# Optimization experiments

Hardware: AMD Instinct MI355X
Metric: run time of the kernel (lower is better)

## Reference

```python
import jax, jax.numpy as jnp
import numpy as np

H = 64
W = 64
MOVES = 15          # ring expansion steps in make_weight_map
THRESHOLD = 5       # self.threshold
BG_WEIGHT = 10.0    # default weight outside the rings


def make_weight_map(kp):
    """Faithful vectorized version of the 15-move ring construction.
    kp = (kp_x, kp_y) int32. A boundary column/row is written once (at the
    first move where the clamped index hits the border) and then the
    left/right/up/down flag stops further writes: write at move m iff
    m <= max(dist_to_border, 1)."""
    kp_x, kp_y = kp[0], kp[1]
    ys = jnp.arange(H)[:, None]
    xs = jnp.arange(W)[None, :]
    wm = jnp.full((H, W), BG_WEIGHT, dtype=jnp.float32)
    m_left = jnp.maximum(kp_x, 1)
    m_right = jnp.maximum(W - 1 - kp_x, 1)
    m_up = jnp.maximum(kp_y, 1)
    m_down = jnp.maximum(H - 1 - kp_y, 1)
    for m in range(1, MOVES + 1):
        xl = jnp.clip(kp_x - m, 0, W - 1)
        xr = jnp.clip(kp_x + m, 0, W - 1)
        yu = jnp.clip(kp_y - m, 0, H - 1)
        yd = jnp.clip(kp_y + m, 0, H - 1)
        w = jnp.float32(0.5 + 0.25 * m)
        col = (((xs == xl) & (m <= m_left)) | ((xs == xr) & (m <= m_right))) \
              & (ys >= yu) & (ys <= yd)
        row = (((ys == yu) & (m <= m_up)) | ((ys == yd) & (m <= m_down))) \
              & (xs >= xl) & (xs <= xr)
        wm = jnp.where(col | row, w, wm)
    return wm


def setup_inputs() -> dict:
    key = jax.random.key(0)
    k1, k2, k3 = jax.random.split(key, 3)
    B, N, C = 64, 17, 32
    keymap_query = jax.random.normal(k1, (B, C, H, W), dtype=jnp.float32)
    memory_keys = jax.random.normal(k2, (B, N, C), dtype=jnp.float32)
    memory_joints = jax.random.randint(k3, (B, N, 2), 0, 64, dtype=jnp.int32)
    return {"keymap_query": keymap_query,
            "memory_keys": memory_keys,
            "memory_joints": memory_joints}


def reference(keymap_query, memory_keys, memory_joints):
    B, C, Hh, Ww = keymap_query.shape
    N = memory_keys.shape[1]
    # per-slot L2 distance over channels: ||q[b,:,y,x] - k[b,n,:]||
    q2 = jnp.sum(keymap_query * keymap_query, axis=1)          # [B,H,W]
    k2 = jnp.sum(memory_keys * memory_keys, axis=-1)           # [B,N]
    dot = jnp.einsum('bchw,bnc->bnhw', keymap_query, memory_keys)
    d2 = q2[:, None] + k2[:, :, None, None] - 2.0 * dot
    dist = jnp.sqrt(jnp.maximum(d2, 0.0))                      # [B,N,H,W]
    # weighted distance (calc_distance with weighted=True)
    wmaps = jax.vmap(jax.vmap(make_weight_map))(memory_joints)  # [B,N,H,W]
    wdist = dist * wmaps
    flat = wdist.reshape(B, N, Hh * Ww)
    min_d = jnp.min(flat, axis=-1)                             # [B,N]
    nonzero = jnp.any(memory_keys != 0, axis=-1)
    # int(torch.min(distance)) > threshold  ->  skip; dist >= 0 so int == floor
    valid = nonzero & (jnp.floor(min_d).astype(jnp.int32) <= THRESHOLD)
    # argmin addressing + crop(keymap, mv, mh, 1, 1) memory update
    idx = jnp.argmin(flat, axis=-1)                            # [B,N]
    kq_flat = keymap_query.reshape(B, C, Hh * Ww)
    gathered = kq_flat[jnp.arange(B)[:, None], :, idx]         # [B,N,C]
    new_keys = jnp.where(valid[..., None], gathered, memory_keys)
    # x4 bilinear refine (align_corners=False semantics) + argmin at 256x256
    dist_x4 = jax.image.resize(wdist, (B, N, 4 * Hh, 4 * Ww), method='bilinear')
    sidx = jnp.argmin(dist_x4.reshape(B, N, -1), axis=-1)
    sv = (sidx // (4 * Ww)).astype(jnp.int32)
    sh = (sidx % (4 * Ww)).astype(jnp.int32)
    joints = jnp.where(valid[..., None], jnp.stack([sv, sh], axis=-1),
                       jnp.int32(-1))                          # (-1,-1) == None
    return joints, valid, new_keys, dist_x4
```

## Files before the change

### kernel.cpp

```cpp
#include <hip/hip_runtime.h>
#include <cfloat>

#define HH 64
#define WW 64
#define NKEYS 17
#define CCH 32
#define BG_W 10.0f

__device__ inline void wave_argmin(float &v, int &i) {
    #pragma unroll
    for (int off = 32; off > 0; off >>= 1) {
        float ov = __shfl_down(v, off, 64);
        int   oi = __shfl_down(i, off, 64);
        if (ov < v || (ov == v && oi < i)) { v = ov; i = oi; }
    }
}

__global__ __launch_bounds__(256) void ee_kernel(
    const float* __restrict__ kq,
    const float* __restrict__ mkeys,
    const int*   __restrict__ mjoints,
    float* __restrict__ out_joints,
    float* __restrict__ out_valid,
    float* __restrict__ out_keys,
    float* __restrict__ out_x4)
{
    const int bid = blockIdx.x;
    const int bn  = (bid & 7) * (NKEYS * 8) + (bid >> 3);
    const int b   = bn / NKEYS;
    const int tid = threadIdx.x;

    __shared__ float s_mk[CCH];
    __shared__ __align__(16) float s_wd[HH * WW];
    __shared__ float s_rv[4];
    __shared__ int   s_ri[4];

    if (tid < CCH) s_mk[tid] = mkeys[bn * CCH + tid];
    __syncthreads();

    float k2 = 0.0f;
    bool  nz = false;
    #pragma unroll
    for (int c = 0; c < CCH; c++) {
        float v = s_mk[c];
        k2 += v * v;
        nz = nz || (v != 0.0f);
    }

    const int kpx = mjoints[bn * 2 + 0];
    const int kpy = mjoints[bn * 2 + 1];
    const int bxc = (kpx == 0) ? 0 : ((kpx == WW - 1) ? WW - 1 : -1);
    const int byc = (kpy == 0) ? 0 : ((kpy == HH - 1) ? HH - 1 : -1);

    const float4* kq4 = (const float4*)(kq + (size_t)b * CCH * HH * WW);

    float bestv = FLT_MAX;
    int   besti = 0;

    for (int j = 0; j < 4; j++) {
        const int chunk = tid + 256 * j;
        float4 dot = make_float4(0.f, 0.f, 0.f, 0.f);
        float4 q2  = make_float4(0.f, 0.f, 0.f, 0.f);
        #pragma unroll
        for (int c = 0; c < CCH; c++) {
            float4 v = kq4[c * 1024 + chunk];
            float  m = s_mk[c];
            dot.x += v.x * m;  dot.y += v.y * m;
            dot.z += v.z * m;  dot.w += v.w * m;
            q2.x  += v.x * v.x; q2.y += v.y * v.y;
            q2.z  += v.z * v.z; q2.w += v.w * v.w;
        }
        float dots[4] = {dot.x, dot.y, dot.z, dot.w};
        float q2s[4]  = {q2.x,  q2.y,  q2.z,  q2.w};
        float4 wd;
        float* wdp = (float*)&wd;
        const int p0 = chunk * 4;
        #pragma unroll
        for (int k = 0; k < 4; k++) {
            const int p  = p0 + k;
            const int px = p & (WW - 1);
            const int py = p >> 6;
            float d2   = (q2s[k] + k2) - 2.0f * dots[k];
            float dist = sqrtf(fmaxf(d2, 0.0f));
            const int adx = abs(px - kpx);
            const int ady = abs(py - kpy);
            int M = 0;
            if (adx <= 15 && ady <= adx) M = adx;
            if (ady <= 15 && adx <= ady) M = max(M, ady);
            if ((px == bxc && ady <= 1) || (py == byc && adx <= 1)) M = max(M, 1);
            float wgt = (M > 0) ? fmaf(0.25f, (float)M, 0.5f) : BG_W;
            float wv = dist * wgt;
            wdp[k] = wv;
            if (wv < bestv) { bestv = wv; besti = p; }
        }
        ((float4*)s_wd)[chunk] = wd;
    }

    __syncthreads();
    wave_argmin(bestv, besti);
    if ((tid & 63) == 0) { s_rv[tid >> 6] = bestv; s_ri[tid >> 6] = besti; }
    __syncthreads();
    if (tid == 0) {
        float v = s_rv[0]; int i0 = s_ri[0];
        for (int w2 = 1; w2 < 4; w2++) {
            float ov = s_rv[w2]; int oi = s_ri[w2];
            if (ov < v || (ov == v && oi < i0)) { v = ov; i0 = oi; }
        }
        s_rv[0] = v; s_ri[0] = i0;
    }
    __syncthreads();
    const float min_d = s_rv[0];
    const int   cbest = s_ri[0];
    const bool  valid = nz && ((int)floorf(min_d) <= 5);

    if (tid < CCH) {
        float o = valid ? kq[(size_t)(b * CCH + tid) * (HH * WW) + cbest] : s_mk[tid];
        out_keys[bn * CCH + tid] = o;
    }

    const int jx   = tid & 63;
    const int yg   = tid >> 6;
    const int jxm1 = max(jx - 1, 0);
    const int jxp1 = min(jx + 1, WW - 1);
    const bool xe0 = (jx == 0);
    const bool xe1 = (jx == WW - 1);

    auto xrow = [&](int cy) -> float4 {
        const float* rr = s_wd + cy * WW;
        const float a  = rr[jxm1];
        const float bb = rr[jx];
        const float c  = rr[jxp1];
        float4 o;
        o.x = xe0 ? bb : fmaf(0.375f, a, 0.625f * bb);
        o.y = xe0 ? bb : fmaf(0.125f, a, 0.875f * bb);
        o.z = xe1 ? bb : fmaf(0.125f, c, 0.875f * bb);
        o.w = xe1 ? bb : fmaf(0.375f, c, 0.625f * bb);
        return o;
    };
    auto lerp4 = [](float wa, const float4& A, float wb, const float4& B) {
        float4 o;
        o.x = fmaf(wa, A.x, wb * B.x);
        o.y = fmaf(wa, A.y, wb * B.y);
        o.z = fmaf(wa, A.z, wb * B.z);
        o.w = fmaf(wa, A.w, wb * B.w);
        return o;
    };

    float fbv = FLT_MAX;
    int   fbi = 0;
    auto upd = [&](float val, int idx) {
        if (val < fbv) { fbv = val; fbi = idx; }
    };

    float4* xo4 = (float4*)(out_x4 + (size_t)bn * (256 * 256)) + jx;

    const int jy0 = yg * 16;
    float4 Xc = xrow(jy0);
    float4 Xp = (jy0 > 0) ? xrow(jy0 - 1) : Xc;

    for (int jy = jy0; jy < jy0 + 16; jy++) {
        const float4 Xn = (jy < HH - 1) ? xrow(jy + 1) : Xc;
        float4 v0, v1, v2, v3;
        if (jy == 0) { v0 = Xc; v1 = Xc; }
        else {
            v0 = lerp4(0.375f, Xp, 0.625f, Xc);
            v1 = lerp4(0.125f, Xp, 0.875f, Xc);
        }
        if (jy == HH - 1) { v2 = Xc; v3 = Xc; }
        else {
            v2 = lerp4(0.875f, Xc, 0.125f, Xn);
            v3 = lerp4(0.625f, Xc, 0.375f, Xn);
        }
        const int r0 = jy * 4;
        xo4[(size_t)(r0 + 0) * 64] = v0;
        xo4[(size_t)(r0 + 1) * 64] = v1;
        xo4[(size_t)(r0 + 2) * 64] = v2;
        xo4[(size_t)(r0 + 3) * 64] = v3;
        const int ib = r0 * 256 + 4 * jx;
        upd(v0.x, ib);       upd(v0.y, ib + 1);   upd(v0.z, ib + 2);   upd(v0.w, ib + 3);
        upd(v1.x, ib + 256); upd(v1.y, ib + 257); upd(v1.z, ib + 258); upd(v1.w, ib + 259);
        upd(v2.x, ib + 512); upd(v2.y, ib + 513); upd(v2.z, ib + 514); upd(v2.w, ib + 515);
        upd(v3.x, ib + 768); upd(v3.y, ib + 769); upd(v3.z, ib + 770); upd(v3.w, ib + 771);
        Xp = Xc;
        Xc = Xn;
    }

    wave_argmin(fbv, fbi);
    __syncthreads();
    if ((tid & 63) == 0) { s_rv[tid >> 6] = fbv; s_ri[tid >> 6] = fbi; }
    __syncthreads();
    if (tid == 0) {
        float v = s_rv[0]; int i0 = s_ri[0];
        for (int w2 = 1; w2 < 4; w2++) {
            float ov = s_rv[w2]; int oi = s_ri[w2];
            if (ov < v || (ov == v && oi < i0)) { v = ov; i0 = oi; }
        }
        int sv, sh;
        if (valid) { sv = i0 >> 8; sh = i0 & 255; }
        else       { sv = -1;      sh = -1;       }
        out_joints[bn * 2 + 0] = (float)sv;
        out_joints[bn * 2 + 1] = (float)sh;
        out_valid[bn] = valid ? 1.0f : 0.0f;
    }
}

extern "C" void kernel_launch(void* const* d_in, const int* in_sizes, int n_in,
                              void* d_out, int out_size, void* d_ws, size_t ws_size,
                              hipStream_t stream) {
    const float* kq = (const float*)d_in[0];
    const float* mk = (const float*)d_in[1];
    const int*   mj = (const int*)d_in[2];

    const int B = in_sizes[1] / (NKEYS * CCH);
    const int BN = B * NKEYS;

    float* out_f     = (float*)d_out;
    float* o_joints  = out_f;
    float* o_valid   = o_joints + BN * 2;
    float* o_keys    = o_valid + BN;
    float* o_x4      = o_keys + BN * CCH;

    ee_kernel<<<dim3(BN), dim3(256), 0, stream>>>(kq, mk, mj, o_joints, o_valid, o_keys, o_x4);
}
```

Baseline: 375.2 us.

## Split each slot across four row-group blocks and finish argmin in a second kernel

The single kernel is split into two. The first runs four blocks per (b,n) slot, each computing an 18-row halo band of the weighted distance map, its 16 rows of bilinear x4 upsampling, and partial coarse and fine argmins written as packed value/index words to workspace. A small second kernel reduces the partials, computes validity, gathers new keys and writes the joints. This raises grid parallelism and shrinks shared memory per block. The cost is that the distance map is recomputed for the two halo rows, and there is an extra kernel launch and a workspace round trip. The fallback of using out_keys as workspace is fragile, and the packed-uint64 min relies on all distances being non-negative.

```diff
diff --git a/kernel.cpp b/kernel.cpp
--- a/kernel.cpp
+++ b/kernel.cpp
@@ -7,6 +7,14 @@
 #define CCH 32
 #define BG_W 10.0f
 
+struct VI { float v; int i; };
+__device__ inline VI vimin(VI a, VI b) { return (b.v < a.v) ? b : a; }
+
+__device__ inline VI row4min(const float4& v, int i0) {
+    VI a = {v.x, i0}, b = {v.y, i0 + 1}, c = {v.z, i0 + 2}, d = {v.w, i0 + 3};
+    return vimin(vimin(a, b), vimin(c, d));
+}
+
 __device__ inline void wave_argmin(float &v, int &i) {
     #pragma unroll
     for (int off = 32; off > 0; off >>= 1) {
@@ -16,22 +24,27 @@
     }
 }
 
-__global__ __launch_bounds__(256) void ee_kernel(
+__device__ inline unsigned long long packvi(float v, int i) {
+    return ((unsigned long long)__float_as_uint(v) << 32) | (unsigned int)i;
+}
+
+__global__ __launch_bounds__(256) void ee_map(
     const float* __restrict__ kq,
     const float* __restrict__ mkeys,
     const int*   __restrict__ mjoints,
-    float* __restrict__ out_joints,
-    float* __restrict__ out_valid,
-    float* __restrict__ out_keys,
-    float* __restrict__ out_x4)
+    float* __restrict__ out_x4,
+    unsigned long long* __restrict__ ws)
 {
+    const int nb  = gridDim.x;
     const int bid = blockIdx.x;
-    const int bn  = (bid & 7) * (NKEYS * 8) + (bid >> 3);
+    const int bnyg = ((nb & 7) == 0) ? ((bid & 7) * (nb >> 3) + (bid >> 3)) : bid;
+    const int bn  = bnyg >> 2;
+    const int yg  = bnyg & 3;
     const int b   = bn / NKEYS;
     const int tid = threadIdx.x;
 
     __shared__ float s_mk[CCH];
-    __shared__ __align__(16) float s_wd[HH * WW];
+    __shared__ __align__(16) float s_wd[18 * WW];
     __shared__ float s_rv[4];
     __shared__ int   s_ri[4];
 
@@ -39,13 +52,8 @@
     __syncthreads();
 
     float k2 = 0.0f;
-    bool  nz = false;
-    #pragma unroll
-    for (int c = 0; c < CCH; c++) {
-        float v = s_mk[c];
-        k2 += v * v;
-        nz = nz || (v != 0.0f);
-    }
+    #pragma unroll
+    for (int c = 0; c < CCH; c++) { float v = s_mk[c]; k2 += v * v; }
 
     const int kpx = mjoints[bn * 2 + 0];
     const int kpy = mjoints[bn * 2 + 1];
@@ -54,51 +62,62 @@
 
     const float4* kq4 = (const float4*)(kq + (size_t)b * CCH * HH * WW);
 
-    float bestv = FLT_MAX;
-    int   besti = 0;
-
-    for (int j = 0; j < 4; j++) {
-        const int chunk = tid + 256 * j;
-        float4 dot = make_float4(0.f, 0.f, 0.f, 0.f);
-        float4 q2  = make_float4(0.f, 0.f, 0.f, 0.f);
-        #pragma unroll
-        for (int c = 0; c < CCH; c++) {
-            float4 v = kq4[c * 1024 + chunk];
-            float  m = s_mk[c];
-            dot.x += v.x * m;  dot.y += v.y * m;
-            dot.z += v.z * m;  dot.w += v.w * m;
-            q2.x  += v.x * v.x; q2.y += v.y * v.y;
-            q2.z  += v.z * v.z; q2.w += v.w * v.w;
-        }
-        float dots[4] = {dot.x, dot.y, dot.z, dot.w};
-        float q2s[4]  = {q2.x,  q2.y,  q2.z,  q2.w};
-        float4 wd;
-        float* wdp = (float*)&wd;
-        const int p0 = chunk * 4;
-        #pragma unroll
-        for (int k = 0; k < 4; k++) {
-            const int p  = p0 + k;
-            const int px = p & (WW - 1);
-            const int py = p >> 6;
-            float d2   = (q2s[k] + k2) - 2.0f * dots[k];
-            float dist = sqrtf(fmaxf(d2, 0.0f));
-            const int adx = abs(px - kpx);
-            const int ady = abs(py - kpy);
-            int M = 0;
-            if (adx <= 15 && ady <= adx) M = adx;
-            if (ady <= 15 && adx <= ady) M = max(M, ady);
-            if ((px == bxc && ady <= 1) || (py == byc && adx <= 1)) M = max(M, 1);
-            float wgt = (M > 0) ? fmaf(0.25f, (float)M, 0.5f) : BG_W;
-            float wv = dist * wgt;
-            wdp[k] = wv;
-            if (wv < bestv) { bestv = wv; besti = p; }
-        }
-        ((float4*)s_wd)[chunk] = wd;
-    }
-
-    __syncthreads();
-    wave_argmin(bestv, besti);
-    if ((tid & 63) == 0) { s_rv[tid >> 6] = bestv; s_ri[tid >> 6] = besti; }
+    VI coarse = {FLT_MAX, 0x7fffffff};
+    const int gy_base = yg * 16 - 1;
+
+    #pragma unroll
+    for (int pass = 0; pass < 2; pass++) {
+        const int chunk = tid + (pass << 8);
+        if (chunk < 288) {
+            const int L  = chunk >> 4;
+            const int cx = chunk & 15;
+            const int gy = gy_base + L;
+            if ((unsigned)gy < (unsigned)HH) {
+                const int gchunk = gy * 16 + cx;
+                float4 dot = make_float4(0.f, 0.f, 0.f, 0.f);
+                float4 q2  = make_float4(0.f, 0.f, 0.f, 0.f);
+                #pragma unroll
+                for (int c = 0; c < CCH; c++) {
+                    float4 v = kq4[c * 1024 + gchunk];
+                    float  m = s_mk[c];
+                    dot.x += v.x * m;  dot.y += v.y * m;
+                    dot.z += v.z * m;  dot.w += v.w * m;
+                    q2.x  += v.x * v.x; q2.y += v.y * v.y;
+                    q2.z  += v.z * v.z; q2.w += v.w * v.w;
+                }
+                float dots[4] = {dot.x, dot.y, dot.z, dot.w};
+                float q2s[4]  = {q2.x,  q2.y,  q2.z,  q2.w};
+                float4 wd;
+                float* wdp = (float*)&wd;
+                const int p0 = gy * WW + cx * 4;
+                #pragma unroll
+                for (int k = 0; k < 4; k++) {
+                    const int px = (cx * 4 + k);
+                    float d2   = (q2s[k] + k2) - 2.0f * dots[k];
+                    float dist = sqrtf(fmaxf(d2, 0.0f));
+                    const int adx = abs(px - kpx);
+                    const int ady = abs(gy - kpy);
+                    int M = 0;
+                    if (adx <= 15 && ady <= adx) M = adx;
+                    if (ady <= 15 && adx <= ady) M = max(M, ady);
+                    if ((px == bxc && ady <= 1) || (gy == byc && adx <= 1)) M = max(M, 1);
+                    float wgt = (M > 0) ? fmaf(0.25f, (float)M, 0.5f) : BG_W;
+                    wdp[k] = dist * wgt;
+                }
+                ((float4*)s_wd)[chunk] = wd;
+                if (L >= 1 && L <= 16) {
+                    coarse = vimin(coarse, row4min(wd, p0));
+                }
+            }
+        }
+    }
+    __syncthreads();
+
+    {
+        float cv = coarse.v; int ci = coarse.i;
+        wave_argmin(cv, ci);
+        if ((tid & 63) == 0) { s_rv[tid >> 6] = cv; s_ri[tid >> 6] = ci; }
+    }
     __syncthreads();
     if (tid == 0) {
         float v = s_rv[0]; int i0 = s_ri[0];
@@ -106,27 +125,18 @@
             float ov = s_rv[w2]; int oi = s_ri[w2];
             if (ov < v || (ov == v && oi < i0)) { v = ov; i0 = oi; }
         }
-        s_rv[0] = v; s_ri[0] = i0;
-    }
-    __syncthreads();
-    const float min_d = s_rv[0];
-    const int   cbest = s_ri[0];
-    const bool  valid = nz && ((int)floorf(min_d) <= 5);
-
-    if (tid < CCH) {
-        float o = valid ? kq[(size_t)(b * CCH + tid) * (HH * WW) + cbest] : s_mk[tid];
-        out_keys[bn * CCH + tid] = o;
+        ws[bn * 8 + yg] = packvi(v, i0);
     }
 
     const int jx   = tid & 63;
-    const int yg   = tid >> 6;
+    const int suby = tid >> 6;
     const int jxm1 = max(jx - 1, 0);
     const int jxp1 = min(jx + 1, WW - 1);
     const bool xe0 = (jx == 0);
     const bool xe1 = (jx == WW - 1);
 
-    auto xrow = [&](int cy) -> float4 {
-        const float* rr = s_wd + cy * WW;
+    auto xrow = [&](int L) -> float4 {
+        const float* rr = s_wd + L * WW;
         const float a  = rr[jxm1];
         const float bb = rr[jx];
         const float c  = rr[jxp1];
@@ -146,20 +156,19 @@
         return o;
     };
 
-    float fbv = FLT_MAX;
-    int   fbi = 0;
-    auto upd = [&](float val, int idx) {
-        if (val < fbv) { fbv = val; fbi = idx; }
-    };
-
+    VI fine = {FLT_MAX, 0x7fffffff};
     float4* xo4 = (float4*)(out_x4 + (size_t)bn * (256 * 256)) + jx;
 
-    const int jy0 = yg * 16;
-    float4 Xc = xrow(jy0);
-    float4 Xp = (jy0 > 0) ? xrow(jy0 - 1) : Xc;
-
-    for (int jy = jy0; jy < jy0 + 16; jy++) {
-        const float4 Xn = (jy < HH - 1) ? xrow(jy + 1) : Xc;
+    const int jy0 = yg * 16 + suby * 4;
+    const int L0  = suby * 4 + 1;
+    float4 Xc = xrow(L0);
+    float4 Xp = xrow(L0 - 1);
+
+    #pragma unroll
+    for (int q = 0; q < 4; q++) {
+        const int jy = jy0 + q;
+        const int L  = L0 + q;
+        const float4 Xn = xrow(L + 1);
         float4 v0, v1, v2, v3;
         if (jy == 0) { v0 = Xc; v1 = Xc; }
         else {
@@ -177,17 +186,21 @@
         xo4[(size_t)(r0 + 2) * 64] = v2;
         xo4[(size_t)(r0 + 3) * 64] = v3;
         const int ib = r0 * 256 + 4 * jx;
-        upd(v0.x, ib);       upd(v0.y, ib + 1);   upd(v0.z, ib + 2);   upd(v0.w, ib + 3);
-        upd(v1.x, ib + 256); upd(v1.y, ib + 257); upd(v1.z, ib + 258); upd(v1.w, ib + 259);
-        upd(v2.x, ib + 512); upd(v2.y, ib + 513); upd(v2.z, ib + 514); upd(v2.w, ib + 515);
-        upd(v3.x, ib + 768); upd(v3.y, ib + 769); upd(v3.z, ib + 770); upd(v3.w, ib + 771);
+        VI a0 = row4min(v0, ib);
+        VI a1 = row4min(v1, ib + 256);
+        VI a2 = row4min(v2, ib + 512);
+        VI a3 = row4min(v3, ib + 768);
+        fine = vimin(fine, vimin(vimin(a0, a1), vimin(a2, a3)));
         Xp = Xc;
         Xc = Xn;
     }
 
-    wave_argmin(fbv, fbi);
-    __syncthreads();
-    if ((tid & 63) == 0) { s_rv[tid >> 6] = fbv; s_ri[tid >> 6] = fbi; }
+    {
+        float fv = fine.v; int fi = fine.i;
+        wave_argmin(fv, fi);
+        __syncthreads();
+        if ((tid & 63) == 0) { s_rv[tid >> 6] = fv; s_ri[tid >> 6] = fi; }
+    }
     __syncthreads();
     if (tid == 0) {
         float v = s_rv[0]; int i0 = s_ri[0];
@@ -195,11 +208,48 @@
             float ov = s_rv[w2]; int oi = s_ri[w2];
             if (ov < v || (ov == v && oi < i0)) { v = ov; i0 = oi; }
         }
-        int sv, sh;
-        if (valid) { sv = i0 >> 8; sh = i0 & 255; }
-        else       { sv = -1;      sh = -1;       }
-        out_joints[bn * 2 + 0] = (float)sv;
-        out_joints[bn * 2 + 1] = (float)sh;
+        ws[bn * 8 + 4 + yg] = packvi(v, i0);
+    }
+}
+
+__global__ __launch_bounds__(64) void ee_fin(
+    const float* __restrict__ kq,
+    const float* __restrict__ mkeys,
+    float* __restrict__ out_joints,
+    float* __restrict__ out_valid,
+    float* __restrict__ out_keys,
+    const unsigned long long* __restrict__ ws)
+{
+    const int bn   = blockIdx.x;
+    const int b    = bn / NKEYS;
+    const int lane = threadIdx.x;
+
+    unsigned long long pc = (lane < 4) ? ws[bn * 8 + lane]     : ~0ull;
+    unsigned long long pf = (lane < 4) ? ws[bn * 8 + 4 + lane] : ~0ull;
+    #pragma unroll
+    for (int off = 1; off <= 2; off <<= 1) {
+        unsigned long long o;
+        o = __shfl_xor(pc, off, 64); if (o < pc) pc = o;
+        o = __shfl_xor(pf, off, 64); if (o < pf) pf = o;
+    }
+    pc = __shfl(pc, 0, 64);
+    pf = __shfl(pf, 0, 64);
+
+    const float min_d = __uint_as_float((unsigned int)(pc >> 32));
+    const int   cbest = (int)(pc & 0xffffffffu);
+
+    const float mv = (lane < CCH) ? mkeys[bn * CCH + lane] : 0.0f;
+    const bool  nz = __any(mv != 0.0f);
+    const bool  valid = nz && ((int)floorf(min_d) <= 5);
+
+    if (lane < CCH) {
+        float o = valid ? kq[(size_t)(b * CCH + lane) * (HH * WW) + cbest] : mv;
+        out_keys[bn * CCH + lane] = o;
+    }
+    if (lane == 0) {
+        const int fi = (int)(pf & 0xffffffffu);
+        out_joints[bn * 2 + 0] = (float)(valid ? (fi >> 8)  : -1);
+        out_joints[bn * 2 + 1] = (float)(valid ? (fi & 255) : -1);
         out_valid[bn] = valid ? 1.0f : 0.0f;
     }
 }
@@ -211,7 +261,7 @@
     const float* mk = (const float*)d_in[1];
     const int*   mj = (const int*)d_in[2];
 
-    const int B = in_sizes[1] / (NKEYS * CCH);
+    const int B  = in_sizes[1] / (NKEYS * CCH);
     const int BN = B * NKEYS;
 
     float* out_f     = (float*)d_out;
@@ -220,5 +270,13 @@
     float* o_keys    = o_valid + BN;
     float* o_x4      = o_keys + BN * CCH;
 
-    ee_kernel<<<dim3(BN), dim3(256), 0, stream>>>(kq, mk, mj, o_joints, o_valid, o_keys, o_x4);
-}
+    unsigned long long* ws;
+    if (ws_size >= (size_t)BN * 8 * sizeof(unsigned long long)) {
+        ws = (unsigned long long*)d_ws;
+    } else {
+        ws = (unsigned long long*)o_keys;
+    }
+
+    ee_map<<<dim3(BN * 4), dim3(256), 0, stream>>>(kq, mk, mj, o_x4, ws);
+    ee_fin<<<dim3(BN), dim3(64), 0, stream>>>(kq, mk, o_joints, o_valid, o_keys, ws);
+}
```

Measured after the change: 344.7 us. 8.1% less time.
